# Kernel optimization log

Measured on AMD Instinct MI355X. Metric: run time of the kernel, lower is better.

The kernel has to match this reference:

```python
import jax, jax.numpy as jnp
import numpy as np

EMBED_DIM = 1024
NUM_HEADS = 16
HEAD_DIM = EMBED_DIM // NUM_HEADS


def setup_inputs() -> dict:
    key = jax.random.key(0)
    ks = jax.random.split(key, 6)
    s = 1.0 / np.sqrt(EMBED_DIM)
    x = jax.random.normal(ks[0], (2, 2048, EMBED_DIM), dtype=jnp.float32)
    Wk = jax.random.uniform(ks[1], (EMBED_DIM, EMBED_DIM), jnp.float32, -s, s)
    Wq = jax.random.uniform(ks[2], (EMBED_DIM, EMBED_DIM), jnp.float32, -s, s)
    Wv = jax.random.uniform(ks[3], (EMBED_DIM, EMBED_DIM), jnp.float32, -s, s)
    Wo = jax.random.uniform(ks[4], (EMBED_DIM, EMBED_DIM), jnp.float32, -s, s)
    bo = jax.random.uniform(ks[5], (EMBED_DIM,), jnp.float32, -s, s)
    return {"x": x, "Wq": Wq, "Wk": Wk, "Wv": Wv, "Wo": Wo, "bo": bo}


def reference(x, Wq, Wk, Wv, Wo, bo):
    b, s, e = x.shape
    h, d = NUM_HEADS, HEAD_DIM
    scale = d ** (-0.5)
    # nn.Linear: y = x @ W.T ; here W stored as [out, in] -> use W.T
    q = (x @ Wq.T).reshape(b, s, h, d).transpose(0, 2, 1, 3)  # b h s d
    k = (x @ Wk.T).reshape(b, s, h, d).transpose(0, 2, 1, 3)
    v = (x @ Wv.T).reshape(b, s, h, d).transpose(0, 2, 1, 3)
    logits = jnp.einsum('bhqd,bhkd->bhqk', q, k) * scale
    attn = jax.nn.softmax(logits, axis=-1)
    out = jnp.einsum('bhqk,bhkd->bhqd', attn, v)
    out = out.transpose(0, 2, 1, 3).reshape(b, s, e)
    return out @ Wo.T + bo
```

## Files before the change

### kernel.cpp

```cpp
#include <hip/hip_runtime.h>
#include <hip/hip_bf16.h>

using short8 = __attribute__((ext_vector_type(8))) short;
using f32x4  = __attribute__((ext_vector_type(4))) float;
using uint4v = __attribute__((ext_vector_type(4))) unsigned;

#if __has_builtin(__builtin_amdgcn_exp2f)
#define EXP2(x) __builtin_amdgcn_exp2f(x)
#else
#define EXP2(x) exp2f(x)
#endif

__device__ __forceinline__ short f2bf(float f) {
    union { float f; unsigned u; } v; v.f = f;
    unsigned r = v.u + 0x7fffu + ((v.u >> 16) & 1u);
    return (short)(r >> 16);
}
__device__ __forceinline__ unsigned pack_trunc(float a, float b) {
    union { float f; unsigned u; } ua, ub; ua.f = a; ub.f = b;
#if __has_builtin(__builtin_amdgcn_perm)
    return __builtin_amdgcn_perm(ub.u, ua.u, 0x07060302u);
#else
    return (ub.u & 0xFFFF0000u) | (ua.u >> 16);
#endif
}
__device__ __forceinline__ void async_copy16(const short* g, short* s) {
    __builtin_amdgcn_global_load_lds(
        (const __attribute__((address_space(1))) void*)g,
        (__attribute__((address_space(3))) void*)s, 16, 0, 0);
}

__global__ __launch_bounds__(256) void cvt_f32_bf16(
    const float* __restrict__ s0, const float* __restrict__ s1,
    const float* __restrict__ s2, const float* __restrict__ s3,
    const float* __restrict__ s4,
    short* __restrict__ d0, short* __restrict__ d1, short* __restrict__ d2,
    short* __restrict__ d3, short* __restrict__ d4,
    int n0, int n1, int n2, int n3, int n4) {
    const float* s; short* d; int n;
    switch (blockIdx.y) {
        case 0: s = s0; d = d0; n = n0; break;
        case 1: s = s1; d = d1; n = n1; break;
        case 2: s = s2; d = d2; n = n2; break;
        case 3: s = s3; d = d3; n = n3; break;
        default: s = s4; d = d4; n = n4; break;
    }
    const int idx = (blockIdx.x * 256 + threadIdx.x) * 4;
    if (idx < n) {
        float4 v = *(const float4*)(s + idx);
        short4 o;
        o.x = f2bf(v.x); o.y = f2bf(v.y); o.z = f2bf(v.z); o.w = f2bf(v.w);
        *(short4*)(d + idx) = o;
    }
}

template <int MODE>
__device__ __forceinline__ void gemm_body(const short* __restrict__ A,
                                          const short* __restrict__ B,
                                          short* __restrict__ C,
                                          float scale,
                                          short* __restrict__ As,
                                          short* __restrict__ Bs) {
    constexpr int Kd = 1024, Nd = 1024, Sd = 2048;

    const int tid  = threadIdx.x;
    const int w    = tid >> 6, lane = tid & 63;
    const int quad = lane >> 4, l16 = lane & 15;
    const int xr   = l16 & 7;
    const int wm   = (w >> 1) * 64, wn = (w & 1) * 64;
    const int bm   = blockIdx.y * 128, bn = blockIdx.x * 128;

    f32x4 acc[4][4];
#pragma unroll
    for (int i = 0; i < 4; ++i)
#pragma unroll
        for (int j = 0; j < 4; ++j) acc[i][j] = (f32x4){0.f, 0.f, 0.f, 0.f};

    for (int k0 = 0; k0 < Kd; k0 += 64) {
        __syncthreads();
#pragma unroll
        for (int c = 0; c < 4; ++c) {
            int li   = c * 256 + tid;
            int row  = li >> 3;
            int gcol = ((li & 7) ^ (row & 7)) * 8;
            async_copy16(A + (size_t)(bm + row) * Kd + k0 + gcol, &As[li * 8]);
            async_copy16(B + (size_t)(bn + row) * Kd + k0 + gcol, &Bs[li * 8]);
        }
        __syncthreads();

#pragma unroll
        for (int kk = 0; kk < 2; ++kk) {
            short8 af[4], bfv[4];
#pragma unroll
            for (int mi = 0; mi < 4; ++mi) {
                const int r = wm + mi * 16 + l16;
                af[mi] = *(const short8*)(
                    &As[r * 64 + (((kk * 4 + quad) ^ xr) * 8)]);
            }
#pragma unroll
            for (int ni = 0; ni < 4; ++ni) {
                const int r = wn + ni * 16 + l16;
                bfv[ni] = *(const short8*)(
                    &Bs[r * 64 + (((kk * 4 + quad) ^ xr) * 8)]);
            }
#pragma unroll
            for (int mi = 0; mi < 4; ++mi)
#pragma unroll
                for (int ni = 0; ni < 4; ++ni) {
                    if constexpr (MODE == 2)
                        acc[mi][ni] = __builtin_amdgcn_mfma_f32_16x16x32_bf16(
                            bfv[ni], af[mi], acc[mi][ni], 0, 0, 0);
                    else
                        acc[mi][ni] = __builtin_amdgcn_mfma_f32_16x16x32_bf16(
                            af[mi], bfv[ni], acc[mi][ni], 0, 0, 0);
                }
        }
    }

    if constexpr (MODE == 2) {
#pragma unroll
        for (int mi = 0; mi < 4; ++mi) {
            const int m_g = bm + wm + mi * 16 + l16;
            const int b_  = m_g >> 11, s_ = m_g & 2047;
#pragma unroll
            for (int ni = 0; ni < 4; ++ni)
#pragma unroll
                for (int r = 0; r < 4; ++r) {
                    const int n_g = bn + wn + ni * 16 + quad * 4 + r;
                    C[(size_t)b_ * Nd * Sd + (size_t)n_g * Sd + s_] =
                        f2bf(acc[mi][ni][r]);
                }
        }
    } else {
#pragma unroll
        for (int ni = 0; ni < 4; ++ni) {
            const int colg = bn + wn + ni * 16 + l16;
#pragma unroll
            for (int mi = 0; mi < 4; ++mi)
#pragma unroll
                for (int r = 0; r < 4; ++r) {
                    const int rowg = bm + wm + mi * 16 + quad * 4 + r;
                    C[(size_t)rowg * Nd + colg] = f2bf(acc[mi][ni][r] * scale);
                }
        }
    }
}

#define CSC 0.18033688f

__global__ __launch_bounds__(256, 3) void proj_gemm(
    const short* __restrict__ X,
    const short* __restrict__ Wq, const short* __restrict__ Wk,
    const short* __restrict__ Wv,
    short* __restrict__ Qo, short* __restrict__ Ko, short* __restrict__ VTo) {
    __shared__ __align__(16) short As[128 * 64];
    __shared__ __align__(16) short Bs[128 * 64];
    if (blockIdx.z == 0)
        gemm_body<0>(X, Wq, Qo, CSC, As, Bs);
    else if (blockIdx.z == 1)
        gemm_body<0>(X, Wk, Ko, 1.0f, As, Bs);
    else
        gemm_body<2>(X, Wv, VTo, 1.0f, As, Bs);
}

__global__ __launch_bounds__(256, 2) void out_gemm(
    const short* __restrict__ A, const short* __restrict__ B,
    const float* __restrict__ bias, float* __restrict__ C) {
    constexpr int Kd = 1024, Nd = 1024;
    __shared__ __align__(16) short As[64 * 64];
    __shared__ __align__(16) short Bs[128 * 64];

    const int tid  = threadIdx.x;
    const int w    = tid >> 6, lane = tid & 63;
    const int quad = lane >> 4, l16 = lane & 15;
    const int xr   = l16 & 7;
    const int wm   = (w >> 1) * 32, wn = (w & 1) * 64;
    const int bm   = blockIdx.y * 64, bn = blockIdx.x * 128;

    f32x4 acc[2][4];
#pragma unroll
    for (int i = 0; i < 2; ++i)
#pragma unroll
        for (int j = 0; j < 4; ++j) acc[i][j] = (f32x4){0.f, 0.f, 0.f, 0.f};

    for (int k0 = 0; k0 < Kd; k0 += 64) {
        __syncthreads();
#pragma unroll
        for (int c = 0; c < 2; ++c) {
            int li   = c * 256 + tid;
            int row  = li >> 3;
            int gcol = ((li & 7) ^ (row & 7)) * 8;
            async_copy16(A + (size_t)(bm + row) * Kd + k0 + gcol, &As[li * 8]);
        }
#pragma unroll
        for (int c = 0; c < 4; ++c) {
            int li   = c * 256 + tid;
            int row  = li >> 3;
            int gcol = ((li & 7) ^ (row & 7)) * 8;
            async_copy16(B + (size_t)(bn + row) * Kd + k0 + gcol, &Bs[li * 8]);
        }
        __syncthreads();

#pragma unroll
        for (int kk = 0; kk < 2; ++kk) {
            short8 af[2], bfv[4];
#pragma unroll
            for (int mi = 0; mi < 2; ++mi) {
                const int r = wm + mi * 16 + l16;
                af[mi] = *(const short8*)(
                    &As[r * 64 + (((kk * 4 + quad) ^ xr) * 8)]);
            }
#pragma unroll
            for (int ni = 0; ni < 4; ++ni) {
                const int r = wn + ni * 16 + l16;
                bfv[ni] = *(const short8*)(
                    &Bs[r * 64 + (((kk * 4 + quad) ^ xr) * 8)]);
            }
#pragma unroll
            for (int mi = 0; mi < 2; ++mi)
#pragma unroll
                for (int ni = 0; ni < 4; ++ni)
                    acc[mi][ni] = __builtin_amdgcn_mfma_f32_16x16x32_bf16(
                        af[mi], bfv[ni], acc[mi][ni], 0, 0, 0);
        }
    }

#pragma unroll
    for (int ni = 0; ni < 4; ++ni) {
        const int colg = bn + wn + ni * 16 + l16;
        const float bv = bias[colg];
#pragma unroll
        for (int mi = 0; mi < 2; ++mi)
#pragma unroll
            for (int r = 0; r < 4; ++r) {
                const int rowg = bm + wm + mi * 16 + quad * 4 + r;
                C[(size_t)rowg * Nd + colg] = acc[mi][ni][r] + bv;
            }
    }
}

__global__ __launch_bounds__(256, 2) void attn_kernel(
    const short* __restrict__ Q, const short* __restrict__ K,
    const short* __restrict__ VT, short* __restrict__ O) {
    constexpr int S = 2048, E = 1024, NT = S / 64;
    __shared__ __align__(16) short Ks[2][64 * 64];
    __shared__ __align__(16) short Vs[2][64 * 64];

    const int tid  = threadIdx.x;
    const int w    = tid >> 6, lane = tid & 63;
    const int quad = lane >> 4, l16 = lane & 15;
    const int bh   = blockIdx.y, b = bh >> 4, h = bh & 15;
    const int qt   = blockIdx.x;

    const int    q0   = qt * 128 + w * 32;
    const size_t base = (size_t)b * S * E;
    const size_t vtb  = (size_t)b * E * S;
    const int    hc   = h * 64;
    const int    xr   = l16 & 7;

    short8 aq[2][2];
#pragma unroll
    for (int qg = 0; qg < 2; ++qg) {
        const short* qp = Q + base + (size_t)(q0 + qg * 16 + l16) * E + hc + quad * 8;
        aq[qg][0] = *(const short8*)(qp);
        aq[qg][1] = *(const short8*)(qp + 32);
    }

    f32x4 oT[2][4], o_sum[2];
#pragma unroll
    for (int qg = 0; qg < 2; ++qg) {
        o_sum[qg] = (f32x4){0.f, 0.f, 0.f, 0.f};
#pragma unroll
        for (int i = 0; i < 4; ++i) oT[qg][i] = (f32x4){0.f, 0.f, 0.f, 0.f};
    }

    int          kdst[2], vdst0[2], vdst1[2];
    const short* kga[2];
    const short* vga[2];
#pragma unroll
    for (int c = 0; c < 2; ++c) {
        int li = c * 256 + tid, row = li >> 3, cc = li & 7;
        kdst[c] = row * 64 + ((cc ^ (row & 7)) * 8);
        int c0   = 4 * (cc >> 2) + 2 * (cc & 1);
        int boff = 4 * ((cc >> 1) & 1);
        vdst0[c] = row * 64 + ((c0 ^ (row & 7)) * 8) + boff;
        vdst1[c] = row * 64 + (((c0 + 1) ^ (row & 7)) * 8) + boff;
        kga[c]   = K + base + (size_t)row * E + hc + cc * 8;
        vga[c]   = VT + vtb + (size_t)(hc + row) * S + cc * 8;
    }

    short8 kr[2], vr[2];
#pragma unroll
    for (int c = 0; c < 2; ++c) {
        kr[c] = *(const short8*)(kga[c]);
        vr[c] = *(const short8*)(vga[c]);
    }
#pragma unroll
    for (int c = 0; c < 2; ++c) {
        *(short8*)(&Ks[0][kdst[c]]) = kr[c];
        short4 lo, hi;
        lo.x = vr[c][0]; lo.y = vr[c][1]; lo.z = vr[c][2]; lo.w = vr[c][3];
        hi.x = vr[c][4]; hi.y = vr[c][5]; hi.z = vr[c][6]; hi.w = vr[c][7];
        *(short4*)(&Vs[0][vdst0[c]]) = lo;
        *(short4*)(&Vs[0][vdst1[c]]) = hi;
    }
#pragma unroll
    for (int c = 0; c < 2; ++c) {
        kr[c] = *(const short8*)(kga[c] + (size_t)64 * E);
        vr[c] = *(const short8*)(vga[c] + 64);
    }
    __syncthreads();

    const short8 ones = (short8){0x3F80, 0x3F80, 0x3F80, 0x3F80,
                                 0x3F80, 0x3F80, 0x3F80, 0x3F80};
    const float  LB   = 0.00281502f;

    for (int kt = 0; kt < NT; ++kt) {
        const int    cur = kt & 1;
        const short* Kc  = Ks[cur];
        const short* Vc  = Vs[cur];

        if (kt + 1 < NT) {
            short* Kn = Ks[cur ^ 1];
            short* Vn = Vs[cur ^ 1];
#pragma unroll
            for (int c = 0; c < 2; ++c) {
                *(short8*)(&Kn[kdst[c]]) = kr[c];
                short4 lo, hi;
                lo.x = vr[c][0]; lo.y = vr[c][1]; lo.z = vr[c][2]; lo.w = vr[c][3];
                hi.x = vr[c][4]; hi.y = vr[c][5]; hi.z = vr[c][6]; hi.w = vr[c][7];
                *(short4*)(&Vn[vdst0[c]]) = lo;
                *(short4*)(&Vn[vdst1[c]]) = hi;
            }
            if (kt + 2 < NT) {
#pragma unroll
                for (int c = 0; c < 2; ++c) {
                    kr[c] = *(const short8*)(kga[c] + (size_t)(kt + 2) * 64 * E);
                    vr[c] = *(const short8*)(vga[c] + (kt + 2) * 64);
                }
            }
        }

        uint4v pkv[2][2];
#pragma unroll
        for (int kn = 0; kn < 4; ++kn) {
            const short* kb  = &Kc[(kn * 16 + l16) * 64];
            short8       bk0 = *(const short8*)(kb + ((quad ^ xr) * 8));
            short8       bk1 = *(const short8*)(kb + (((quad + 4) ^ xr) * 8));
#pragma unroll
            for (int qg = 0; qg < 2; ++qg) {
                f32x4 a = (f32x4){LB, LB, LB, LB};
                a = __builtin_amdgcn_mfma_f32_16x16x32_bf16(bk0, aq[qg][0], a, 0, 0, 0);
                a = __builtin_amdgcn_mfma_f32_16x16x32_bf16(bk1, aq[qg][1], a, 0, 0, 0);
                pkv[qg][kn >> 1][(kn & 1) * 2]     = pack_trunc(EXP2(a[0]), EXP2(a[1]));
                pkv[qg][kn >> 1][(kn & 1) * 2 + 1] = pack_trunc(EXP2(a[2]), EXP2(a[3]));
            }
        }

#pragma unroll
        for (int ks = 0; ks < 2; ++ks) {
            short8 pf[2];
#pragma unroll
            for (int qg = 0; qg < 2; ++qg) {
                union { uint4v u; short8 s; } cv;
                cv.u   = pkv[qg][ks];
                pf[qg] = cv.s;
                o_sum[qg] = __builtin_amdgcn_mfma_f32_16x16x32_bf16(
                    ones, pf[qg], o_sum[qg], 0, 0, 0);
            }
#pragma unroll
            for (int ni = 0; ni < 4; ++ni) {
                const int rv = ni * 16 + l16;
                short8 vb =
                    *(const short8*)(&Vc[rv * 64 + (((ks * 4 + quad) ^ xr) * 8)]);
#pragma unroll
                for (int qg = 0; qg < 2; ++qg)
                    oT[qg][ni] = __builtin_amdgcn_mfma_f32_16x16x32_bf16(
                        vb, pf[qg], oT[qg][ni], 0, 0, 0);
            }
        }
        __syncthreads();
    }

#pragma unroll
    for (int qg = 0; qg < 2; ++qg) {
        const float inv = 1.0f / o_sum[qg][0];
        const int   qg_ = q0 + qg * 16 + l16;
#pragma unroll
        for (int ni = 0; ni < 4; ++ni) {
            short4 ov;
            ov.x = f2bf(oT[qg][ni][0] * inv);
            ov.y = f2bf(oT[qg][ni][1] * inv);
            ov.z = f2bf(oT[qg][ni][2] * inv);
            ov.w = f2bf(oT[qg][ni][3] * inv);
            *(short4*)(&O[base + (size_t)qg_ * E + hc + ni * 16 + quad * 4]) = ov;
        }
    }
}

extern "C" void kernel_launch(void* const* d_in, const int* in_sizes, int n_in,
                              void* d_out, int out_size, void* d_ws, size_t ws_size,
                              hipStream_t stream) {
    const float* x  = (const float*)d_in[0];
    const float* Wq = (const float*)d_in[1];
    const float* Wk = (const float*)d_in[2];
    const float* Wv = (const float*)d_in[3];
    const float* Wo = (const float*)d_in[4];
    const float* bo = (const float*)d_in[5];
    float* out = (float*)d_out;

    constexpr int XN = 2 * 2048 * 1024;
    constexpr int WN = 1024 * 1024;

    short* Xb  = (short*)d_ws;
    short* Wqb = Xb + XN;
    short* Wkb = Wqb + WN;
    short* Wvb = Wkb + WN;
    short* Wob = Wvb + WN;
    short* Qb  = Wob + WN;
    short* Kb  = Qb + XN;
    short* VTb = Kb + XN;

    cvt_f32_bf16<<<dim3(4096, 5), 256, 0, stream>>>(
        x, Wq, Wk, Wv, Wo, Xb, Wqb, Wkb, Wvb, Wob, XN, WN, WN, WN, WN);
    proj_gemm<<<dim3(8, 32, 3), 256, 0, stream>>>(Xb, Wqb, Wkb, Wvb, Qb, Kb, VTb);
    attn_kernel<<<dim3(16, 32), 256, 0, stream>>>(Qb, Kb, VTb, Xb );
    out_gemm<<<dim3(8, 64), 256, 0, stream>>>(Xb, Wob, bo, out);
}
```

Baseline: 169.6 us.

## Deepen attention K/V prefetch, add XCD-aware block mapping, trim conversion grid

The attention kernel's K/V staging becomes a two-tile-ahead register prefetch with two register sets, unrolled by two so the loop handles both LDS buffers with fixed indices. The MFMA section is wrapped in s_setprio to favour compute waves. Blocks are remapped from a 2D grid to a 1D grid so that all query tiles of a head land on the same XCD, which should improve L2 reuse of K/V. The conversion kernel drops its idle blocks (the old 4096x5 grid ran many empty weight blocks) and its bounds checks. In exchange, the extra register set raises register pressure, and the code assumes NT is even.

Result: no change. 171.2 us (+1.0%).

```diff
diff --git a/kernel.cpp b/kernel.cpp
--- a/kernel.cpp
+++ b/kernel.cpp
@@ -35,23 +35,26 @@
     const float* __restrict__ s2, const float* __restrict__ s3,
     const float* __restrict__ s4,
     short* __restrict__ d0, short* __restrict__ d1, short* __restrict__ d2,
-    short* __restrict__ d3, short* __restrict__ d4,
-    int n0, int n1, int n2, int n3, int n4) {
-    const float* s; short* d; int n;
-    switch (blockIdx.y) {
-        case 0: s = s0; d = d0; n = n0; break;
-        case 1: s = s1; d = d1; n = n1; break;
-        case 2: s = s2; d = d2; n = n2; break;
-        case 3: s = s3; d = d3; n = n3; break;
-        default: s = s4; d = d4; n = n4; break;
-    }
-    const int idx = (blockIdx.x * 256 + threadIdx.x) * 4;
-    if (idx < n) {
-        float4 v = *(const float4*)(s + idx);
-        short4 o;
-        o.x = f2bf(v.x); o.y = f2bf(v.y); o.z = f2bf(v.z); o.w = f2bf(v.w);
-        *(short4*)(d + idx) = o;
-    }
+    short* __restrict__ d3, short* __restrict__ d4) {
+    const int bid = blockIdx.x;
+    const float* s; short* d; int base;
+    if (bid < 4096) {
+        s = s0; d = d0; base = bid << 10;
+    } else {
+        const int r = bid - 4096;
+        base = (r & 1023) << 10;
+        switch (r >> 10) {
+            case 0: s = s1; d = d1; break;
+            case 1: s = s2; d = d2; break;
+            case 2: s = s3; d = d3; break;
+            default: s = s4; d = d4; break;
+        }
+    }
+    const int idx = base + threadIdx.x * 4;
+    float4 v = *(const float4*)(s + idx);
+    short4 o;
+    o.x = f2bf(v.x); o.y = f2bf(v.y); o.z = f2bf(v.z); o.w = f2bf(v.w);
+    *(short4*)(d + idx) = o;
 }
 
 template <int MODE>
@@ -249,8 +252,12 @@
     const int tid  = threadIdx.x;
     const int w    = tid >> 6, lane = tid & 63;
     const int quad = lane >> 4, l16 = lane & 15;
-    const int bh   = blockIdx.y, b = bh >> 4, h = bh & 15;
-    const int qt   = blockIdx.x;
+
+    const int bid  = blockIdx.x;
+    const int xcd  = bid & 7, slot = bid >> 3;
+    const int qt   = slot & 15;
+    const int bh   = xcd + ((slot >> 4) << 3);
+    const int b    = bh >> 4, h = bh & 15;
 
     const int    q0   = qt * 128 + w * 32;
     const size_t base = (size_t)b * S * E;
@@ -289,58 +296,34 @@
         vga[c]   = VT + vtb + (size_t)(hc + row) * S + cc * 8;
     }
 
-    short8 kr[2], vr[2];
-#pragma unroll
-    for (int c = 0; c < 2; ++c) {
-        kr[c] = *(const short8*)(kga[c]);
-        vr[c] = *(const short8*)(vga[c]);
-    }
-#pragma unroll
-    for (int c = 0; c < 2; ++c) {
-        *(short8*)(&Ks[0][kdst[c]]) = kr[c];
-        short4 lo, hi;
-        lo.x = vr[c][0]; lo.y = vr[c][1]; lo.z = vr[c][2]; lo.w = vr[c][3];
-        hi.x = vr[c][4]; hi.y = vr[c][5]; hi.z = vr[c][6]; hi.w = vr[c][7];
-        *(short4*)(&Vs[0][vdst0[c]]) = lo;
-        *(short4*)(&Vs[0][vdst1[c]]) = hi;
-    }
-#pragma unroll
-    for (int c = 0; c < 2; ++c) {
-        kr[c] = *(const short8*)(kga[c] + (size_t)64 * E);
-        vr[c] = *(const short8*)(vga[c] + 64);
-    }
-    __syncthreads();
+    short8 krA[2], vrA[2], krB[2], vrB[2];
+
+    auto load_regs = [&](short8* krX, short8* vrX, int t) {
+#pragma unroll
+        for (int c = 0; c < 2; ++c) {
+            krX[c] = *(const short8*)(kga[c] + (size_t)t * 64 * E);
+            vrX[c] = *(const short8*)(vga[c] + t * 64);
+        }
+    };
+    auto store_regs = [&](short* Kn, short* Vn, const short8* krX,
+                          const short8* vrX) {
+#pragma unroll
+        for (int c = 0; c < 2; ++c) {
+            *(short8*)(&Kn[kdst[c]]) = krX[c];
+            short4 lo, hi;
+            lo.x = vrX[c][0]; lo.y = vrX[c][1]; lo.z = vrX[c][2]; lo.w = vrX[c][3];
+            hi.x = vrX[c][4]; hi.y = vrX[c][5]; hi.z = vrX[c][6]; hi.w = vrX[c][7];
+            *(short4*)(&Vn[vdst0[c]]) = lo;
+            *(short4*)(&Vn[vdst1[c]]) = hi;
+        }
+    };
 
     const short8 ones = (short8){0x3F80, 0x3F80, 0x3F80, 0x3F80,
                                  0x3F80, 0x3F80, 0x3F80, 0x3F80};
     const float  LB   = 0.00281502f;
 
-    for (int kt = 0; kt < NT; ++kt) {
-        const int    cur = kt & 1;
-        const short* Kc  = Ks[cur];
-        const short* Vc  = Vs[cur];
-
-        if (kt + 1 < NT) {
-            short* Kn = Ks[cur ^ 1];
-            short* Vn = Vs[cur ^ 1];
-#pragma unroll
-            for (int c = 0; c < 2; ++c) {
-                *(short8*)(&Kn[kdst[c]]) = kr[c];
-                short4 lo, hi;
-                lo.x = vr[c][0]; lo.y = vr[c][1]; lo.z = vr[c][2]; lo.w = vr[c][3];
-                hi.x = vr[c][4]; hi.y = vr[c][5]; hi.z = vr[c][6]; hi.w = vr[c][7];
-                *(short4*)(&Vn[vdst0[c]]) = lo;
-                *(short4*)(&Vn[vdst1[c]]) = hi;
-            }
-            if (kt + 2 < NT) {
-#pragma unroll
-                for (int c = 0; c < 2; ++c) {
-                    kr[c] = *(const short8*)(kga[c] + (size_t)(kt + 2) * 64 * E);
-                    vr[c] = *(const short8*)(vga[c] + (kt + 2) * 64);
-                }
-            }
-        }
-
+    auto compute_tile = [&](const short* Kc, const short* Vc) {
+        __builtin_amdgcn_s_setprio(1);
         uint4v pkv[2][2];
 #pragma unroll
         for (int kn = 0; kn < 4; ++kn) {
@@ -379,6 +362,25 @@
                         vb, pf[qg], oT[qg][ni], 0, 0, 0);
             }
         }
+        __builtin_amdgcn_s_setprio(0);
+    };
+
+    load_regs(krA, vrA, 0);
+    store_regs(Ks[0], Vs[0], krA, vrA);
+    load_regs(krA, vrA, 1);
+    load_regs(krB, vrB, 2);
+    __syncthreads();
+
+#pragma unroll 1
+    for (int kt = 0; kt < NT; kt += 2) {
+        store_regs(Ks[1], Vs[1], krA, vrA);
+        if (kt + 3 < NT) load_regs(krA, vrA, kt + 3);
+        compute_tile(Ks[0], Vs[0]);
+        __syncthreads();
+
+        if (kt + 2 < NT) store_regs(Ks[0], Vs[0], krB, vrB);
+        if (kt + 4 < NT) load_regs(krB, vrB, kt + 4);
+        compute_tile(Ks[1], Vs[1]);
         __syncthreads();
     }
 
@@ -421,9 +423,9 @@
     short* Kb  = Qb + XN;
     short* VTb = Kb + XN;
 
-    cvt_f32_bf16<<<dim3(4096, 5), 256, 0, stream>>>(
-        x, Wq, Wk, Wv, Wo, Xb, Wqb, Wkb, Wvb, Wob, XN, WN, WN, WN, WN);
+    cvt_f32_bf16<<<dim3(8192), 256, 0, stream>>>(
+        x, Wq, Wk, Wv, Wo, Xb, Wqb, Wkb, Wvb, Wob);
     proj_gemm<<<dim3(8, 32, 3), 256, 0, stream>>>(Xb, Wqb, Wkb, Wvb, Qb, Kb, VTb);
-    attn_kernel<<<dim3(16, 32), 256, 0, stream>>>(Qb, Kb, VTb, Xb );
+    attn_kernel<<<dim3(512), 256, 0, stream>>>(Qb, Kb, VTb, Xb );
     out_gemm<<<dim3(8, 64), 256, 0, stream>>>(Xb, Wob, bo, out);
 }
```
